# Kernel optimization log

Hardware: AMD Instinct MI355X
Metric: run time of the kernel (lower is better)

## Reference

```python
import jax, jax.numpy as jnp
import numpy as np

B, L, E, H, W = 2, 8192, 1024, 16, 128
HD = E // H  # 64


def setup_inputs() -> dict:
    key = jax.random.key(0)
    ks = jax.random.split(key, 9)
    s = 1.0 / np.sqrt(E)
    inp = {"x": jax.random.normal(ks[0], (B, L, E), jnp.float32)}
    for i, n in enumerate(["Wq", "Wk", "Wv", "Wo"]):
        inp[n] = jax.random.uniform(ks[1 + i], (E, E), jnp.float32, -s, s)
    for i, n in enumerate(["bq", "bk", "bv", "bo"]):
        inp[n] = jax.random.uniform(ks[5 + i], (E,), jnp.float32, -s, s)
    return inp


def _skew_prob(p, w):
    # (..., w, 2w+1) -> (..., w, 3w) with row i right-shifted by i:
    # out[..., i, i+j] = p[..., i, j]  (zeros elsewhere)
    lead = p.shape[:-2]
    M, Lc = p.shape[-2], p.shape[-1]
    p = jnp.pad(p, [(0, 0)] * len(lead) + [(0, 0), (0, M + 1)])
    p = p.reshape(*lead, M * (Lc + M + 1))[..., :-M].reshape(*lead, M, M + Lc)
    return p[..., :-1]


def _sliding_attend(q, k, v, w):
    # q,k,v: (b,h,l,d); banded attention, window w on each side (2w+1 diagonals)
    b, h, l, d = q.shape
    c = l // w
    qc = q.reshape(b, h, c, w, d)
    # per-chunk key/value windows of 3w tokens (w halo each side, zero padded)
    idx = jnp.arange(c)[:, None] * w + jnp.arange(3 * w)[None, :]  # (c, 3w)
    kw = jnp.pad(k, ((0, 0), (0, 0), (w, w), (0, 0)))[:, :, idx]  # (b,h,c,3w,d)
    s = jnp.einsum('bhcqd,bhckd->bhcqk', qc, kw)  # (b,h,c,w,3w)
    # extract band: band[i, j] = s[i, i+j], j in [0, 2w] (offset d = j - w)
    gidx = (jnp.arange(w)[:, None] + jnp.arange(2 * w + 1)[None, :])[None, None, None]
    band = jnp.take_along_axis(s, gidx, axis=-1).reshape(b, h, l, 2 * w + 1)
    # mask out-of-range positions (matches the module's edge -inf loop)
    pos = jnp.arange(l)[:, None] + (jnp.arange(2 * w + 1) - w)[None, :]
    band = jnp.where((pos >= 0) & (pos < l), band, -jnp.inf)
    prob = jax.nn.softmax(band / np.sqrt(d), axis=-1)  # scale by sqrt(head_dim)
    vw = jnp.pad(v, ((0, 0), (0, 0), (w, w), (0, 0)))[:, :, idx]  # (b,h,c,3w,d)
    p3 = _skew_prob(prob.reshape(b, h, c, w, 2 * w + 1), w)  # (b,h,c,w,3w)
    ctx = jnp.einsum('bhcqk,bhckd->bhcqd', p3, vw)
    return ctx.reshape(b, h, l, d)


def reference(x, Wq, Wk, Wv, Wo, bq, bk, bv, bo):
    q = (x @ Wq.T + bq).reshape(B, L, H, HD).transpose(0, 2, 1, 3)
    k = (x @ Wk.T + bk).reshape(B, L, H, HD).transpose(0, 2, 1, 3)
    v = (x @ Wv.T + bv).reshape(B, L, H, HD).transpose(0, 2, 1, 3)
    ctx = _sliding_attend(q, k, v, W)
    ctx = ctx.transpose(0, 2, 1, 3).reshape(B, L, E)
    return ctx @ Wo.T + bo
```

## Files before the change

### kernel.cpp

```cpp
#include <hip/hip_runtime.h>
#include <math.h>

#define B_SZ  2
#define L_SEQ 8192
#define EMB   1024
#define NH    16
#define HDIM  64
#define WIN   128
#define MROWS (B_SZ*L_SEQ)

typedef __attribute__((ext_vector_type(8))) _Float16 f16x8;
typedef __attribute__((ext_vector_type(4))) _Float16 f16x4;
typedef __attribute__((ext_vector_type(4))) float f32x4;

__device__ __forceinline__ void gload16(const void* g, void* l) {
    __builtin_amdgcn_global_load_lds(
        (const __attribute__((address_space(1))) unsigned int*)g,
        (__attribute__((address_space(3))) unsigned int*)l, 16, 0, 0);
}

__global__ __launch_bounds__(256)
void round_all(const float* __restrict__ x,
               const float* __restrict__ wq, const float* __restrict__ wk,
               const float* __restrict__ wv, const float* __restrict__ wo,
               _Float16* __restrict__ xf, _Float16* __restrict__ q16,
               _Float16* __restrict__ k16, _Float16* __restrict__ v16,
               _Float16* __restrict__ o16)
{
    const size_t NX = (size_t)MROWS * EMB, NW = (size_t)EMB * EMB;
    size_t gid = ((size_t)blockIdx.x * 256 + threadIdx.x) * 4;
    const float* src; _Float16* dst; size_t off;
    if (gid < NX)               { src = x;  dst = xf;  off = gid; }
    else if (gid < NX + NW)     { src = wq; dst = q16; off = gid - NX; }
    else if (gid < NX + 2*NW)   { src = wk; dst = k16; off = gid - NX - 2*NW + NW; }
    else if (gid < NX + 3*NW)   { src = wv; dst = v16; off = gid - NX - 2*NW; }
    else                        { src = wo; dst = o16; off = gid - NX - 3*NW; }
    float4 v = *(const float4*)(src + off);
    f16x4 o;
    o[0] = (_Float16)v.x; o[1] = (_Float16)v.y;
    o[2] = (_Float16)v.z; o[3] = (_Float16)v.w;
    *(f16x4*)(dst + off) = o;
}


#define STAGE_HT(ptr_, tb_, op_, h_, kt_)                                      \
    {                                                                          \
        char* d_ = smem + (op_) * 65536 + ((kt_) & 1) * 32768 + (h_) * 16384 + ldst; \
        const _Float16* s_ = (ptr_) + ((size_t)((tb_) + (h_) * 128 + srow6)) * 1024 + (kt_) * 64 + gch; \
        gload16(s_, d_);                                                       \
        gload16(s_ + 64 * 1024, d_ + 8192);                                    \
    }

#define DSREAD_A(qr_)                                                          \
    _Pragma("unroll")                                                          \
    for (int i_ = 0; i_ < 4; ++i_) {                                           \
        const int ro_ = (qr_) * 8192 + (i_ * 16 + frow) * 128;                 \
        af[i_][0] = *(const f16x8*)(Ab + ro_ + sb0);                           \
        af[i_][1] = *(const f16x8*)(Ab + ro_ + sb1);                           \
    }

#define DSREAD_B(qc_)                                                          \
    _Pragma("unroll")                                                          \
    for (int j_ = 0; j_ < 2; ++j_) {                                           \
        const int ro_ = (brow + (qc_) * 32 + j_ * 16 + frow) * 128;            \
        bf[j_][0] = *(const f16x8*)(Bb + ro_ + sb0);                           \
        bf[j_][1] = *(const f16x8*)(Bb + ro_ + sb1);                           \
    }

#define MFMA16(qr_, qc_)                                                       \
    __builtin_amdgcn_s_setprio(1);                                             \
    _Pragma("unroll")                                                          \
    for (int ks_ = 0; ks_ < 2; ++ks_)                                          \
        _Pragma("unroll")                                                      \
        for (int i_ = 0; i_ < 4; ++i_)                                         \
            _Pragma("unroll")                                                  \
            for (int j_ = 0; j_ < 2; ++j_)                                     \
                acc[(qr_) * 4 + i_][(qc_) * 2 + j_] =                          \
                    __builtin_amdgcn_mfma_f32_16x16x32_f16(                    \
                        af[i_][ks_], bf[j_][ks_],                              \
                        acc[(qr_) * 4 + i_][(qc_) * 2 + j_], 0, 0, 0);         \
    __builtin_amdgcn_s_setprio(0);

#define BARM()                                                                 \
    asm volatile("" ::: "memory");                                             \
    __builtin_amdgcn_s_barrier();                                              \
    asm volatile("" ::: "memory");

#define GEMM8_CORE(Aptr, Bptr)                                                 \
    const int t = threadIdx.x;                                                 \
    const int wave = t >> 6, lane = t & 63;                                    \
    const int wr = wave >> 2, wc = wave & 3;                                   \
    const int frow = lane & 15, quad = lane >> 4;                              \
    const int srow6 = t >> 3;                                                  \
    const int gch = ((t & 7) ^ (srow6 & 7)) * 8;                               \
    const int ldst = t * 16;                                                   \
    const int sb0 = (quad ^ (frow & 7)) * 16, sb1 = sb0 ^ 64;                  \
    const int brow = (wc & 1) * 64;                                            \
    f32x4 acc[8][4] = {};                                                      \
    f16x8 af[4][2], bf[2][2];                                                  \
    STAGE_HT(Aptr, bm, 0, 0, 0) STAGE_HT(Aptr, bm, 0, 1, 0)                    \
    STAGE_HT(Bptr, bn, 1, 0, 0) STAGE_HT(Bptr, bn, 1, 1, 0)                    \
    asm volatile("s_waitcnt vmcnt(0)" ::: "memory");                           \
    BARM()                                                                     \
    for (int kt = 0; kt < 16; ++kt) {                                          \
        const char* Ab = smem + (kt & 1) * 32768 + wr * 16384;                 \
        const char* Bb = smem + 65536 + (kt & 1) * 32768 + (wc >> 1) * 16384;  \
                            \
        DSREAD_A(0) DSREAD_B(0)                                                \
        if (kt < 15) {                                                         \
            STAGE_HT(Aptr, bm, 0, 0, kt + 1)                                   \
            STAGE_HT(Aptr, bm, 0, 1, kt + 1)                                   \
        }                                                                      \
        BARM()                                                                 \
        MFMA16(0, 0)                                                           \
        BARM()                                                                 \
                              \
        DSREAD_B(1)                                                            \
        if (kt < 15) {                                                         \
            STAGE_HT(Bptr, bn, 1, 0, kt + 1)                                   \
            STAGE_HT(Bptr, bn, 1, 1, kt + 1)                                   \
        }                                                                      \
        BARM()                                                                 \
        MFMA16(0, 1)                                                           \
        BARM()                                                                 \
                                                      \
        DSREAD_A(1)                                                            \
        BARM()                                                                 \
        MFMA16(1, 1)                                                           \
        BARM()                                                                 \
          \
        DSREAD_B(0)                                                            \
        if (kt < 15) asm volatile("s_waitcnt vmcnt(0)" ::: "memory");          \
        BARM()                                                                 \
        MFMA16(1, 0)                                                           \
        BARM()                                                                 \
    }

__global__ __launch_bounds__(512, 2)
void gemm_qkv(const _Float16* __restrict__ X,
              const _Float16* __restrict__ Wq, const _Float16* __restrict__ Wk,
              const _Float16* __restrict__ Wv,
              const float* __restrict__ bq, const float* __restrict__ bk,
              const float* __restrict__ bv,
              _Float16* __restrict__ qf, _Float16* __restrict__ kf,
              _Float16* __restrict__ vtf)
{
    __shared__ __attribute__((aligned(16))) char smem[131072];

    const int id = blockIdx.x;
    const int row = (id / 96) * 8 + (id & 7);
    const int colq = (id >> 3) % 12;
    const int wsel = colq >> 2;
    const int bm = row * 256, bn = (colq & 3) * 256;
    const _Float16* Bw = wsel == 0 ? Wq : wsel == 1 ? Wk : Wv;
    const float* bias = wsel == 0 ? bq : wsel == 1 ? bk : bv;
    const float scale = wsel == 0 ? 0.125f : 1.0f;

    GEMM8_CORE(X, Bw)

    char* Cw = smem + wave * 8192;
    const int bb = bm >> 13;
    const int l0 = (bm & (L_SEQ - 1)) + wr * 128;
    const int h = (bn >> 6) + wc;
    if (wsel < 2) {
        _Float16* dst = wsel == 0 ? qf : kf;
        const size_t hb = ((size_t)(bb * NH + h)) * L_SEQ * HDIM;
        #pragma unroll
        for (int ih = 0; ih < 2; ++ih) {
            asm volatile("" ::: "memory");
            #pragma unroll
            for (int i = 0; i < 4; ++i)
                #pragma unroll
                for (int j = 0; j < 4; ++j) {
                    const int lc = j * 16 + frow;
                    const float bvv = bias[bn + wc * 64 + lc];
                    #pragma unroll
                    for (int r = 0; r < 4; ++r) {
                        const int lr = i * 16 + quad * 4 + r;
                        const int bo = lr * 128 + ((lc * 2) ^ ((lr & 7) << 4));
                        *(_Float16*)(Cw + bo) = (_Float16)((acc[ih * 4 + i][j][r] + bvv) * scale);
                    }
                }
            asm volatile("" ::: "memory");
            #pragma unroll
            for (int p = 0; p < 8; ++p) {
                const int idx = p * 64 + lane;
                const int lr = idx >> 3, seg = idx & 7;
                const int bo = lr * 128 + ((seg * 16) ^ ((lr & 7) << 4));
                uint4 v = *(const uint4*)(Cw + bo);
                *(uint4*)&dst[hb + (size_t)(l0 + ih * 64 + lr) * HDIM + seg * 8] = v;
            }
        }
    } else {
        const size_t hb = ((size_t)(bb * NH + h)) * HDIM * L_SEQ;
        #pragma unroll
        for (int ih = 0; ih < 2; ++ih) {
            asm volatile("" ::: "memory");
            #pragma unroll
            for (int i = 0; i < 4; ++i)
                #pragma unroll
                for (int j = 0; j < 4; ++j) {
                    const int lc = j * 16 + frow;
                    const float bvv = bias[bn + wc * 64 + lc];
                    #pragma unroll
                    for (int r = 0; r < 4; ++r) {
                        const int lr = i * 16 + quad * 4 + r;
                        const int bo = lc * 128 + ((lr * 2) ^ ((lc & 7) << 4));
                        *(_Float16*)(Cw + bo) = (_Float16)(acc[ih * 4 + i][j][r] + bvv);
                    }
                }
            asm volatile("" ::: "memory");
            #pragma unroll
            for (int p = 0; p < 8; ++p) {
                const int idx = p * 64 + lane;
                const int dc = idx >> 3, sl = idx & 7;
                const int bo = dc * 128 + ((sl * 16) ^ ((dc & 7) << 4));
                uint4 v = *(const uint4*)(Cw + bo);
                *(uint4*)&vtf[hb + (size_t)dc * L_SEQ + (l0 + ih * 64 + sl * 8)] = v;
            }
        }
    }
}

__global__ __launch_bounds__(512, 2)
void gemm_out(const _Float16* __restrict__ A, const _Float16* __restrict__ Bwm,
              const float* __restrict__ bias, float* __restrict__ C)
{
    constexpr int N = EMB;
    __shared__ __attribute__((aligned(16))) char smem[131072];

    const int id = blockIdx.x;
    const int row = (id / 32) * 8 + (id & 7);
    const int bm = row * 256, bn = ((id >> 3) & 3) * 256;

    GEMM8_CORE(A, Bwm)

    #pragma unroll
    for (int i = 0; i < 8; ++i) {
        int m0 = bm + wr * 128 + i * 16 + quad * 4;
        #pragma unroll
        for (int j = 0; j < 4; ++j) {
            int n = bn + wc * 64 + j * 16 + frow;
            float bvv = bias[n];
            #pragma unroll
            for (int r = 0; r < 4; ++r)
                C[(size_t)(m0 + r) * N + n] = acc[i][j][r] + bvv;
        }
    }
}

__global__ __launch_bounds__(256)
void attn_mfma(const _Float16* __restrict__ qf, const _Float16* __restrict__ kf,
               const _Float16* __restrict__ vtf, _Float16* __restrict__ cf)
{
    __shared__ _Float16 Kf[2][4096], Vf[2][4096];
    __shared__ _Float16 Ps[4][16 * 72];

    const int t = threadIdx.x;
    const int wave = t >> 6, lane = t & 63;
    const int col = lane & 15, quad = lane >> 4;
    const int bh = blockIdx.y;
    const int q0 = blockIdx.x * 128;

    f16x8 qfr[2][2];
    #pragma unroll
    for (int g = 0; g < 2; g++) {
        size_t qidx = ((size_t)bh * L_SEQ + q0 + g * 64 + wave * 16 + col) * HDIM + quad * 8;
        qfr[g][0] = *(const f16x8*)(qf + qidx);
        qfr[g][1] = *(const f16x8*)(qf + qidx + 32);
    }

    f32x4 o[2][4] = {};
    float lsum[2][4] = {};

    const int srow = t >> 3, sc = t & 7;
    _Float16* Pw = Ps[wave];

    const int ktlo = (q0 == 0) ? 2 : 0;
    const int kthi = (q0 == L_SEQ - 128) ? 4 : 6;

#define STAGE_KV(kt_, bsel_)                                                   \
    {                                                                          \
        const int p0s = q0 - WIN + (kt_) * 64;                                 \
        _Pragma("unroll")                                                      \
        for (int sw2 = 0; sw2 < 2; sw2++) {                                    \
            int rowk = sw2 * 32 + srow;                                        \
            int gq = sc ^ (rowk & 7);                                          \
            size_t kgi = ((size_t)bh * L_SEQ + p0s + rowk) * HDIM + gq * 8;    \
            size_t vgi = ((size_t)bh * HDIM + rowk) * L_SEQ + p0s + gq * 8;    \
            int lb = sw2 * 4096 + wave * 1024;                                 \
            gload16(kf + kgi, (char*)&Kf[bsel_][0] + lb);                      \
            gload16(vtf + vgi, (char*)&Vf[bsel_][0] + lb);                     \
        }                                                                      \
    }

    STAGE_KV(ktlo, 0)

    for (int kt = ktlo; kt < kthi; kt++) {
        const int p0 = q0 - WIN + kt * 64;
        const int rel = kt * 64 - WIN;
        const int cb = (kt - ktlo) & 1;
        if (kt + 1 < kthi) {
            STAGE_KV(kt + 1, cb ^ 1)
            asm volatile("s_waitcnt vmcnt(4)" ::: "memory");
        } else {
            asm volatile("s_waitcnt vmcnt(0)" ::: "memory");
        }
        __builtin_amdgcn_s_barrier();
        asm volatile("" ::: "memory");

        const char* Kb = (const char*)&Kf[cb][0];
        const char* Vb = (const char*)&Vf[cb][0];

        #pragma unroll
        for (int g = 0; g < 2; g++) {
            const int oo = g * 64 + wave * 16;
            if (rel < oo - 191 || rel > oo + 143) continue;
            f32x4 s[4] = {};
            #pragma unroll
            for (int ks = 0; ks < 2; ks++)
                #pragma unroll
                for (int n = 0; n < 4; n++) {
                    int off = (n * 16 + col) * 128 + (((ks * 4 + quad) ^ (col & 7)) * 16);
                    f16x8 kfr = *(const f16x8*)(Kb + off);
                    s[n] = __builtin_amdgcn_mfma_f32_16x16x32_f16(qfr[g][ks], kfr, s[n], 0, 0, 0);
                }
            const int rowb = q0 + oo + quad * 4;
            #pragma unroll
            for (int n = 0; n < 4; n++)
                #pragma unroll
                for (int r = 0; r < 4; r++) {
                    int dlt = (p0 + n * 16 + col) - (rowb + r);
                    if (dlt < -WIN || dlt > WIN) s[n][r] = -3e38f;
                }
            #pragma unroll
            for (int n = 0; n < 4; n++)
                #pragma unroll
                for (int r = 0; r < 4; r++) {
                    float pv = __expf(s[n][r]);
                    lsum[g][r] += pv;
                    Pw[(quad * 4 + r) * 72 + n * 16 + col] = (_Float16)pv;
                }
            #pragma unroll
            for (int ks = 0; ks < 2; ks++) {
                f16x8 pfr = *(const f16x8*)&Pw[col * 72 + ks * 32 + quad * 8];
                #pragma unroll
                for (int n = 0; n < 4; n++) {
                    int off = (n * 16 + col) * 128 + (((ks * 4 + quad) ^ (col & 7)) * 16);
                    f16x8 vfr = *(const f16x8*)(Vb + off);
                    o[g][n] = __builtin_amdgcn_mfma_f32_16x16x32_f16(pfr, vfr, o[g][n], 0, 0, 0);
                }
            }
        }
        asm volatile("" ::: "memory");
        __builtin_amdgcn_s_barrier();
        asm volatile("" ::: "memory");
    }

    #pragma unroll
    for (int g = 0; g < 2; g++)
        #pragma unroll
        for (int x = 1; x < 16; x <<= 1)
            #pragma unroll
            for (int r = 0; r < 4; r++)
                lsum[g][r] += __shfl_xor(lsum[g][r], x, 64);

    const int b = bh >> 4, h = bh & 15;
    #pragma unroll
    for (int g = 0; g < 2; g++)
        #pragma unroll
        for (int r = 0; r < 4; r++) {
            float inv = 1.0f / lsum[g][r];
            int q = q0 + g * 64 + wave * 16 + quad * 4 + r;
            size_t base = ((size_t)b * L_SEQ + q) * EMB + h * HDIM;
            #pragma unroll
            for (int n = 0; n < 4; n++)
                cf[base + n * 16 + col] = (_Float16)(o[g][n][r] * inv);
        }
}

extern "C" void kernel_launch(void* const* d_in, const int* in_sizes, int n_in,
                              void* d_out, int out_size, void* d_ws, size_t ws_size,
                              hipStream_t stream) {
    const float* x  = (const float*)d_in[0];
    const float* Wq = (const float*)d_in[1];
    const float* Wk = (const float*)d_in[2];
    const float* Wv = (const float*)d_in[3];
    const float* Wo = (const float*)d_in[4];
    const float* bq = (const float*)d_in[5];
    const float* bk = (const float*)d_in[6];
    const float* bv = (const float*)d_in[7];
    const float* bo = (const float*)d_in[8];
    float* out = (float*)d_out;

    const size_t per = (size_t)B_SZ * NH * L_SEQ * HDIM;
    _Float16* w16 = (_Float16*)d_ws;
    _Float16* xf   = w16;
    _Float16* qf   = w16 + per;
    _Float16* kf   = w16 + 2 * per;
    _Float16* vtf  = w16 + 3 * per;
    _Float16* cf   = w16 + 4 * per;
    _Float16* wq16 = w16 + 5 * per;
    _Float16* wk16 = wq16 + 1048576;
    _Float16* wv16 = wq16 + 2 * 1048576;
    _Float16* wo16 = wq16 + 3 * 1048576;

    const int nround = (MROWS * EMB + 4 * EMB * EMB) / 1024;
    round_all<<<nround, dim3(256), 0, stream>>>(x, Wq, Wk, Wv, Wo, xf, wq16, wk16, wv16, wo16);

    gemm_qkv<<<768, dim3(512), 0, stream>>>(xf, wq16, wk16, wv16, bq, bk, bv, qf, kf, vtf);

    attn_mfma<<<dim3(L_SEQ / 128, B_SZ * NH), dim3(256), 0, stream>>>(qf, kf, vtf, cf);

    gemm_out<<<256, dim3(512), 0, stream>>>(cf, wo16, bo, out);
}
```

Measured before the change: 335.9 us.

## Replace double-buffered K=64 GEMM mainloop with 4-slot K=32 ring pipeline

Both GEMM kernels now use a 4-deep ring of K=32 shared-memory slots, prefetching three stages ahead with partial vmcnt waits, in place of the double-buffered K=64 loop with quadrant-split reads. Each step issues a single MFMA batch per barrier pair and reads the next slot's fragments right after computing. The aim is to hide global-load latency better and cut the number of barriers per K step. In exchange there are more, smaller K iterations and a new XOR swizzle pattern that has to stay bank-conflict free.

```diff
diff --git a/kernel.cpp b/kernel.cpp
--- a/kernel.cpp
+++ b/kernel.cpp
@@ -43,42 +43,33 @@
 }
 
 
-#define STAGE_HT(ptr_, tb_, op_, h_, kt_)                                      \
+#define STAGE32(ptr_, tb_, opb_, kt_, slot_)                                   \
     {                                                                          \
-        char* d_ = smem + (op_) * 65536 + ((kt_) & 1) * 32768 + (h_) * 16384 + ldst; \
-        const _Float16* s_ = (ptr_) + ((size_t)((tb_) + (h_) * 128 + srow6)) * 1024 + (kt_) * 64 + gch; \
+        char* d_ = smem + (opb_) + (slot_) * 16384 + t * 16;                   \
+        const _Float16* s_ = (ptr_) + (size_t)((tb_) + srow4) * 1024           \
+                             + (kt_) * 32 + gch32;                             \
         gload16(s_, d_);                                                       \
-        gload16(s_ + 64 * 1024, d_ + 8192);                                    \
-    }
-
-#define DSREAD_A(qr_)                                                          \
-    _Pragma("unroll")                                                          \
-    for (int i_ = 0; i_ < 4; ++i_) {                                           \
-        const int ro_ = (qr_) * 8192 + (i_ * 16 + frow) * 128;                 \
-        af[i_][0] = *(const f16x8*)(Ab + ro_ + sb0);                           \
-        af[i_][1] = *(const f16x8*)(Ab + ro_ + sb1);                           \
-    }
-
-#define DSREAD_B(qc_)                                                          \
-    _Pragma("unroll")                                                          \
-    for (int j_ = 0; j_ < 2; ++j_) {                                           \
-        const int ro_ = (brow + (qc_) * 32 + j_ * 16 + frow) * 128;            \
-        bf[j_][0] = *(const f16x8*)(Bb + ro_ + sb0);                           \
-        bf[j_][1] = *(const f16x8*)(Bb + ro_ + sb1);                           \
-    }
-
-#define MFMA16(qr_, qc_)                                                       \
+        gload16(s_ + 128 * 1024, d_ + 8192);                                   \
+    }
+
+#define READS32(slot_)                                                         \
+    {                                                                          \
+        const char* Ab_ = smem + (slot_) * 16384;                              \
+        const char* Bb_ = smem + 65536 + (slot_) * 16384;                      \
+        _Pragma("unroll")                                                      \
+        for (int m_ = 0; m_ < 8; ++m_) af[m_] = *(const f16x8*)(Ab_ + aoff[m_]); \
+        _Pragma("unroll")                                                      \
+        for (int n_ = 0; n_ < 4; ++n_) bf[n_] = *(const f16x8*)(Bb_ + boff[n_]); \
+    }
+
+#define MFMA32()                                                               \
     __builtin_amdgcn_s_setprio(1);                                             \
     _Pragma("unroll")                                                          \
-    for (int ks_ = 0; ks_ < 2; ++ks_)                                          \
+    for (int m_ = 0; m_ < 8; ++m_)                                             \
         _Pragma("unroll")                                                      \
-        for (int i_ = 0; i_ < 4; ++i_)                                         \
-            _Pragma("unroll")                                                  \
-            for (int j_ = 0; j_ < 2; ++j_)                                     \
-                acc[(qr_) * 4 + i_][(qc_) * 2 + j_] =                          \
-                    __builtin_amdgcn_mfma_f32_16x16x32_f16(                    \
-                        af[i_][ks_], bf[j_][ks_],                              \
-                        acc[(qr_) * 4 + i_][(qc_) * 2 + j_], 0, 0, 0);         \
+        for (int n_ = 0; n_ < 4; ++n_)                                         \
+            acc[m_][n_] = __builtin_amdgcn_mfma_f32_16x16x32_f16(              \
+                af[m_], bf[n_], acc[m_][n_], 0, 0, 0);                         \
     __builtin_amdgcn_s_setprio(0);
 
 #define BARM()                                                                 \
@@ -86,55 +77,62 @@
     __builtin_amdgcn_s_barrier();                                              \
     asm volatile("" ::: "memory");
 
-#define GEMM8_CORE(Aptr, Bptr)                                                 \
+#define RING_BODY(Aptr, Bptr, kt_, u_)                                         \
+    STAGE32(Aptr, bm, 0, (kt_) + 3, ((u_) + 3) & 3)                            \
+    STAGE32(Bptr, bn, 65536, (kt_) + 3, ((u_) + 3) & 3)                        \
+    asm volatile("s_waitcnt vmcnt(8)" ::: "memory");                           \
+    BARM()                                                                     \
+    MFMA32()                                                                   \
+    READS32(((u_) + 1) & 3)                                                    \
+    BARM()
+
+#define GEMM_RING_CORE(Aptr, Bptr)                                             \
     const int t = threadIdx.x;                                                 \
     const int wave = t >> 6, lane = t & 63;                                    \
     const int wr = wave >> 2, wc = wave & 3;                                   \
     const int frow = lane & 15, quad = lane >> 4;                              \
-    const int srow6 = t >> 3;                                                  \
-    const int gch = ((t & 7) ^ (srow6 & 7)) * 8;                               \
-    const int ldst = t * 16;                                                   \
-    const int sb0 = (quad ^ (frow & 7)) * 16, sb1 = sb0 ^ 64;                  \
-    const int brow = (wc & 1) * 64;                                            \
+    const int srow4 = t >> 2;                                                  \
+    const int gch32 = ((t & 3) ^ ((t >> 3) & 3)) * 8;                          \
+    const int swsl = (quad ^ ((frow >> 1) & 3)) * 16;                          \
+    int aoff[8], boff[4];                                                      \
+    _Pragma("unroll")                                                          \
+    for (int m_ = 0; m_ < 8; ++m_)                                             \
+        aoff[m_] = wr * 8192 + (m_ * 16 + frow) * 64 + swsl;                   \
+    _Pragma("unroll")                                                          \
+    for (int n_ = 0; n_ < 4; ++n_)                                             \
+        boff[n_] = wc * 4096 + (n_ * 16 + frow) * 64 + swsl;                   \
     f32x4 acc[8][4] = {};                                                      \
-    f16x8 af[4][2], bf[2][2];                                                  \
-    STAGE_HT(Aptr, bm, 0, 0, 0) STAGE_HT(Aptr, bm, 0, 1, 0)                    \
-    STAGE_HT(Bptr, bn, 1, 0, 0) STAGE_HT(Bptr, bn, 1, 1, 0)                    \
+    f16x8 af[8], bf[4];                                                        \
+    STAGE32(Aptr, bm, 0, 0, 0) STAGE32(Bptr, bn, 65536, 0, 0)                  \
+    STAGE32(Aptr, bm, 0, 1, 1) STAGE32(Bptr, bn, 65536, 1, 1)                  \
+    STAGE32(Aptr, bm, 0, 2, 2) STAGE32(Bptr, bn, 65536, 2, 2)                  \
+    asm volatile("s_waitcnt vmcnt(4)" ::: "memory");                           \
+    BARM()                                                                     \
+    READS32(0)                                                                 \
+    for (int k4 = 0; k4 < 7; ++k4) {                                           \
+        const int kb = k4 * 4;                                                 \
+        RING_BODY(Aptr, Bptr, kb + 0, 0)                                       \
+        RING_BODY(Aptr, Bptr, kb + 1, 1)                                       \
+        RING_BODY(Aptr, Bptr, kb + 2, 2)                                       \
+        RING_BODY(Aptr, Bptr, kb + 3, 3)                                       \
+    }                                                                          \
+                                 \
+    RING_BODY(Aptr, Bptr, 28, 0)                                               \
+                                                        \
+    asm volatile("s_waitcnt vmcnt(4)" ::: "memory");                           \
+    BARM()                                                                     \
+    MFMA32()                                                                   \
+    READS32(2)                                                                 \
+    BARM()                                                                     \
+                                                        \
     asm volatile("s_waitcnt vmcnt(0)" ::: "memory");                           \
     BARM()                                                                     \
-    for (int kt = 0; kt < 16; ++kt) {                                          \
-        const char* Ab = smem + (kt & 1) * 32768 + wr * 16384;                 \
-        const char* Bb = smem + 65536 + (kt & 1) * 32768 + (wc >> 1) * 16384;  \
-                            \
-        DSREAD_A(0) DSREAD_B(0)                                                \
-        if (kt < 15) {                                                         \
-            STAGE_HT(Aptr, bm, 0, 0, kt + 1)                                   \
-            STAGE_HT(Aptr, bm, 0, 1, kt + 1)                                   \
-        }                                                                      \
-        BARM()                                                                 \
-        MFMA16(0, 0)                                                           \
-        BARM()                                                                 \
-                              \
-        DSREAD_B(1)                                                            \
-        if (kt < 15) {                                                         \
-            STAGE_HT(Bptr, bn, 1, 0, kt + 1)                                   \
-            STAGE_HT(Bptr, bn, 1, 1, kt + 1)                                   \
-        }                                                                      \
-        BARM()                                                                 \
-        MFMA16(0, 1)                                                           \
-        BARM()                                                                 \
-                                                      \
-        DSREAD_A(1)                                                            \
-        BARM()                                                                 \
-        MFMA16(1, 1)                                                           \
-        BARM()                                                                 \
-          \
-        DSREAD_B(0)                                                            \
-        if (kt < 15) asm volatile("s_waitcnt vmcnt(0)" ::: "memory");          \
-        BARM()                                                                 \
-        MFMA16(1, 0)                                                           \
-        BARM()                                                                 \
-    }
+    MFMA32()                                                                   \
+    READS32(3)                                                                 \
+    BARM()                                                                     \
+                                                                    \
+    MFMA32()                                                                   \
+    BARM()
 
 __global__ __launch_bounds__(512, 2)
 void gemm_qkv(const _Float16* __restrict__ X,
@@ -156,7 +154,7 @@
     const float* bias = wsel == 0 ? bq : wsel == 1 ? bk : bv;
     const float scale = wsel == 0 ? 0.125f : 1.0f;
 
-    GEMM8_CORE(X, Bw)
+    GEMM_RING_CORE(X, Bw)
 
     char* Cw = smem + wave * 8192;
     const int bb = bm >> 13;
@@ -233,7 +231,7 @@
     const int row = (id / 32) * 8 + (id & 7);
     const int bm = row * 256, bn = ((id >> 3) & 3) * 256;
 
-    GEMM8_CORE(A, Bwm)
+    GEMM_RING_CORE(A, Bwm)
 
     #pragma unroll
     for (int i = 0; i < 8; ++i) {
```

After: 343.0 us. 2.1% more time.
